# Kernel optimization log

Measured on AMD Instinct MI355X. Metric: run time of the kernel, lower is better.

Reference implementation:

```python
import jax, jax.numpy as jnp
import numpy as np

B, N, K = 32, 8192, 40


def _pi(x, w, b):
    # permute_invariant_layer: subtract per-(sample,feature) max over set dim,
    # then 1x1 conv1d (pointwise matmul over feature dim).
    x = x - jnp.max(x, axis=2, keepdims=True)          # [B, F, N]
    return jnp.einsum('bfn,of->bon', x, w) + b[None, :, None]


def setup_inputs() -> dict:
    key = jax.random.key(0)
    ks = jax.random.split(key, 12)
    def glorot(k, shape, fan_in):
        return jax.random.normal(k, shape, jnp.float32) * (1.0 / np.sqrt(fan_in))
    return {
        'x': jax.random.normal(ks[0], (B, 3, N), jnp.float32),
        'w1': glorot(ks[1], (64, 3), 3),   'b1': jnp.zeros((64,), jnp.float32),
        'w2': glorot(ks[2], (128, 64), 64), 'b2': jnp.zeros((128,), jnp.float32),
        'w3': glorot(ks[3], (256, 128), 128), 'b3': jnp.zeros((256,), jnp.float32),
        'fc1_w': glorot(ks[4], (128, 256), 256), 'fc1_b': jnp.zeros((128,), jnp.float32),
        'fc2_w': glorot(ks[5], (K, 128), 128),   'fc2_b': jnp.zeros((K,), jnp.float32),
    }


def reference(x, w1, b1, w2, b2, w3, b3, fc1_w, fc1_b, fc2_w, fc2_b):
    h = jnp.tanh(_pi(x, w1, b1))          # [B, 64, N]
    h = jnp.tanh(_pi(h, w2, b2))          # [B, 128, N]
    h = jnp.tanh(_pi(h, w3, b3))          # [B, 256, N]
    g = jnp.max(h, axis=2)                # global max pool -> [B, 256]
    # dropout omitted (deterministic/eval reference)
    g = jnp.tanh(g @ fc1_w.T + fc1_b)     # [B, 128]
    g = jnp.tanh(g @ fc2_w.T + fc2_b)     # [B, K]
    return jax.nn.log_softmax(g, axis=-1)
```

## Files before the change

kernel.cpp:

```cpp
#include <hip/hip_runtime.h>
#include <hip/hip_bf16.h>

#define B_  32
#define N_  8192
#define C1  64
#define C2  128
#define C3  256
#define KO  40
#define SLOTS 8

typedef __attribute__((ext_vector_type(8))) short bh8;
typedef __attribute__((ext_vector_type(4))) float f32x4;

union FragU { uint u[4]; bh8 h; uint4 v; };

#define MFMA_BF16 __builtin_amdgcn_mfma_f32_16x16x32_bf16


__device__ __forceinline__ float ftanh(float x) {
    float e = __expf(2.0f * x);
    float r = __builtin_amdgcn_rcpf(e + 1.0f);
    return fmaf(-2.0f, r, 1.0f);
}

__device__ __forceinline__ float quadMax(float v) {
    v = fmaxf(v, __shfl_xor(v, 1, 64));
    v = fmaxf(v, __shfl_xor(v, 2, 64));
    v = fmaxf(v, __shfl_xor(v, 4, 64));
    v = fmaxf(v, __shfl_xor(v, 8, 64));
    return v;
}

__device__ __forceinline__ unsigned encf(float f) {
    unsigned u = __float_as_uint(f);
    return (u & 0x80000000u) ? ~u : (u | 0x80000000u);
}
__device__ __forceinline__ float decf(unsigned e) {
    return __uint_as_float((e & 0x80000000u) ? (e & 0x7fffffffu) : ~e);
}

__device__ __forceinline__ unsigned packbf(float a, float b) {
    __hip_bfloat162 p = __float22bfloat162_rn(make_float2(a, b));
    unsigned u;
    __builtin_memcpy(&u, &p, 4);
    return u;
}


__global__ __launch_bounds__(128) void k_scan(const float* __restrict__ x,
                                              const float* __restrict__ w1,
                                              const float* __restrict__ w2,
                                              const float* __restrict__ w3,
                                              float* __restrict__ mx1p,
                                              float* __restrict__ mx2p,
                                              uint4* __restrict__ w2f,
                                              uint4* __restrict__ w3f,
                                              unsigned* __restrict__ zeroBase) {
    int t = threadIdx.x;
    int bid = blockIdx.x;
    if (bid < 256) {
        int b = bid >> 3, s = bid & 7;
        const float* xb = x + (size_t)b * 3 * N_ + s * 1024 + t;
        float x0[8], x1[8], x2[8];
#pragma unroll
        for (int i = 0; i < 8; ++i) {
            x0[i] = xb[i * 128];
            x1[i] = xb[N_ + i * 128];
            x2[i] = xb[2 * N_ + i * 128];
        }
        float c0 = x0[0], c1 = x1[0], c2 = x2[0];
#pragma unroll
        for (int i = 1; i < 8; ++i) {
            c0 = fmaxf(c0, x0[i]);
            c1 = fmaxf(c1, x1[i]);
            c2 = fmaxf(c2, x2[i]);
        }
        __shared__ float tl[67][132];
#pragma unroll
        for (int o = 0; o < C1; ++o) {
            float w0 = w1[o * 3 + 0], wa = w1[o * 3 + 1], wb = w1[o * 3 + 2];
            float m = -1e30f;
#pragma unroll
            for (int i = 0; i < 8; ++i)
                m = fmaxf(m, fmaf(x0[i], w0, fmaf(x1[i], wa, x2[i] * wb)));
            tl[o][t] = m;
        }
        tl[64][t] = c0;
        tl[65][t] = c1;
        tl[66][t] = c2;
        __syncthreads();
        if (t < 67) {
            const float4* row = (const float4*)&tl[t][0];
            float4 a0 = row[0], a1 = row[1], a2 = row[2], a3 = row[3];
#pragma unroll
            for (int j = 4; j < 32; j += 4) {
                float4 r0 = row[j], r1 = row[j + 1], r2 = row[j + 2], r3 = row[j + 3];
                a0.x = fmaxf(a0.x, r0.x); a0.y = fmaxf(a0.y, r0.y);
                a0.z = fmaxf(a0.z, r0.z); a0.w = fmaxf(a0.w, r0.w);
                a1.x = fmaxf(a1.x, r1.x); a1.y = fmaxf(a1.y, r1.y);
                a1.z = fmaxf(a1.z, r1.z); a1.w = fmaxf(a1.w, r1.w);
                a2.x = fmaxf(a2.x, r2.x); a2.y = fmaxf(a2.y, r2.y);
                a2.z = fmaxf(a2.z, r2.z); a2.w = fmaxf(a2.w, r2.w);
                a3.x = fmaxf(a3.x, r3.x); a3.y = fmaxf(a3.y, r3.y);
                a3.z = fmaxf(a3.z, r3.z); a3.w = fmaxf(a3.w, r3.w);
            }
            float m = fmaxf(fmaxf(fmaxf(a0.x, a0.y), fmaxf(a0.z, a0.w)),
                            fmaxf(fmaxf(a1.x, a1.y), fmaxf(a1.z, a1.w)));
            m = fmaxf(m, fmaxf(fmaxf(a2.x, a2.y), fmaxf(a2.z, a2.w)));
            m = fmaxf(m, fmaxf(fmaxf(a3.x, a3.y), fmaxf(a3.z, a3.w)));
            if (t < 64) mx2p[(s * 32 + b) * 64 + t] = m;
            else        mx1p[(s * 32 + b) * 4 + (t - 64)] = m;
        }
    } else if (bid < 296) {
        int tid = (bid - 256) * 128 + t;
        const float* src;
        uint4* dst;
        if (tid < 1024) {
            int lane = tid & 63, ks = (tid >> 6) & 1, mt = tid >> 7;
            src = w2 + (mt * 16 + (lane & 15)) * C1 + ks * 32 + (lane >> 4) * 8;
            dst = w2f + tid;
        } else {
            int fj = tid - 1024;
            int lane = fj & 63, ks = (fj >> 6) & 3, mt = fj >> 8;
            src = w3 + (mt * 16 + (lane & 15)) * C2 + ks * 32 + (lane >> 4) * 8;
            dst = w3f + fj;
        }
        uint4 o;
        o.x = packbf(src[0], src[1]);
        o.y = packbf(src[2], src[3]);
        o.z = packbf(src[4], src[5]);
        o.w = packbf(src[6], src[7]);
        *dst = o;
    } else {
        int idx = (bid - 296) * 128 + t;
        for (int i = idx; i < 8192 + 4096; i += 256) zeroBase[i] = 0u;
    }
}


__global__ __launch_bounds__(512) void k_passD(const float* __restrict__ x,
                                               const float* __restrict__ w1,
                                               const float* __restrict__ b1,
                                               const float* __restrict__ w2,
                                               const float* __restrict__ b2,
                                               const float* __restrict__ mx1p,
                                               const float* __restrict__ mx2p,
                                               const uint4* __restrict__ w2f,
                                               const uint4* __restrict__ w3f,
                                               unsigned* __restrict__ mx3e,
                                               unsigned* __restrict__ genc) {
    __shared__ uint4 h1v[8][130];
    __shared__ uint2 h2u[32][130];
    __shared__ float w1s[192];
    __shared__ float beff1s[C1];
    __shared__ float m2s[C1];
    __shared__ float beff2s[C2];

    int b = blockIdx.x >> 5;
    int chunk = blockIdx.x & 31;
    int t = threadIdx.x;
    int p = t & 127, hh = t >> 7;
    int lane = t & 63, wv = t >> 6, qd = lane >> 4, ln = lane & 15;

    const float* xbase = x + (size_t)b * 3 * N_ + chunk * 256 + p;
    float xq0[2], xq1[2], xq2[2];
#pragma unroll
    for (int tile = 0; tile < 2; ++tile) {
        xq0[tile] = xbase[tile * 128];
        xq1[tile] = xbase[N_ + tile * 128];
        xq2[tile] = xbase[2 * N_ + tile * 128];
    }

    if (t < 192) w1s[t] = w1[t];
    if (t < C1) {
        float mraw = -1e30f;
#pragma unroll
        for (int s = 0; s < SLOTS; ++s)
            mraw = fmaxf(mraw, mx2p[(s * 32 + b) * 64 + t]);
        float s0 = -1e30f, s1 = -1e30f, s2 = -1e30f;
#pragma unroll
        for (int s = 0; s < SLOTS; ++s) {
            s0 = fmaxf(s0, mx1p[(s * 32 + b) * 4 + 0]);
            s1 = fmaxf(s1, mx1p[(s * 32 + b) * 4 + 1]);
            s2 = fmaxf(s2, mx1p[(s * 32 + b) * 4 + 2]);
        }
        float be = b1[t] - s0 * w1[t * 3 + 0] - s1 * w1[t * 3 + 1]
                         - s2 * w1[t * 3 + 2];
        beff1s[t] = be;
        m2s[t] = ftanh(mraw + be);
    }
    bh8 wf2[2];
    bh8 wf3[2][4];
#pragma unroll
    for (int ks = 0; ks < 2; ++ks) {
        FragU fu;
        fu.v = w2f[(wv * 2 + ks) * 64 + lane];
        wf2[ks] = fu.h;
    }
#pragma unroll
    for (int mi = 0; mi < 2; ++mi)
#pragma unroll
        for (int ks = 0; ks < 4; ++ks) {
            FragU fu;
            fu.v = w3f[((2 * wv + mi) * 4 + ks) * 64 + lane];
            wf3[mi][ks] = fu.h;
        }
    __syncthreads();

    if (t < C2) {
        float a = b2[t];
#pragma unroll 8
        for (int f = 0; f < C1; ++f) a -= m2s[f] * w2[t * C1 + f];
        beff2s[t] = a;
    }

    float vmax2[4];
    float vmax3[2][4];
#pragma unroll
    for (int r = 0; r < 4; ++r) vmax2[r] = -1e30f;
#pragma unroll
    for (int mi = 0; mi < 2; ++mi)
#pragma unroll
        for (int r = 0; r < 4; ++r) vmax3[mi][r] = -1e30f;
    f32x4 bb2;
    bool haveBb2 = false;

    for (int tile = 0; tile < 2; ++tile) {
        float x0 = xq0[tile], x1 = xq1[tile], x2 = xq2[tile];
#pragma unroll
        for (int qq = 0; qq < 2; ++qq) {
            int c = hh * 16 + qq * 8;
            float v[8];
#pragma unroll
            for (int s = 0; s < 8; ++s) {
                float a = beff1s[c + s];
                a = fmaf(x0, w1s[(c + s) * 3 + 0], a);
                a = fmaf(x1, w1s[(c + s) * 3 + 1], a);
                a = fmaf(x2, w1s[(c + s) * 3 + 2], a);
                v[s] = ftanh(a);
            }
            uint4 pk;
            pk.x = packbf(v[0], v[1]);
            pk.y = packbf(v[2], v[3]);
            pk.z = packbf(v[4], v[5]);
            pk.w = packbf(v[6], v[7]);
            h1v[hh * 2 + qq][p] = pk;
        }
        __syncthreads();

        if (!haveBb2) {
#pragma unroll
            for (int r = 0; r < 4; ++r)
                bb2[r] = beff2s[wv * 16 + qd * 4 + r];
            haveBb2 = true;
        }

        for (int nb = 0; nb < 8; ++nb) {
            int n = nb * 16 + ln;
            f32x4 acc = bb2;
#pragma unroll
            for (int ks = 0; ks < 2; ++ks) {
                FragU fb;
                fb.v = h1v[ks * 4 + qd][n];
                acc = MFMA_BF16(wf2[ks], fb.h, acc, 0, 0, 0);
            }
#pragma unroll
            for (int r = 0; r < 4; ++r)
                vmax2[r] = fmaxf(vmax2[r], acc[r]);
            h2u[wv * 4 + qd][n] = make_uint2(packbf(ftanh(acc[0]), ftanh(acc[1])),
                                            packbf(ftanh(acc[2]), ftanh(acc[3])));
        }
        __syncthreads();

        for (int nb = 0; nb < 8; ++nb) {
            int n = nb * 16 + ln;
            f32x4 acc[2];
#pragma unroll
            for (int mi = 0; mi < 2; ++mi) acc[mi] = (f32x4){0.f, 0.f, 0.f, 0.f};
#pragma unroll
            for (int ks = 0; ks < 4; ++ks) {
                int kk = ks * 4 + qd;
                uint2 u0 = h2u[2 * kk][n], u1 = h2u[2 * kk + 1][n];
                FragU fb;
                fb.u[0] = u0.x; fb.u[1] = u0.y; fb.u[2] = u1.x; fb.u[3] = u1.y;
#pragma unroll
                for (int mi = 0; mi < 2; ++mi)
                    acc[mi] = MFMA_BF16(wf3[mi][ks], fb.h, acc[mi], 0, 0, 0);
            }
#pragma unroll
            for (int mi = 0; mi < 2; ++mi)
#pragma unroll
                for (int r = 0; r < 4; ++r)
                    vmax3[mi][r] = fmaxf(vmax3[mi][r], acc[mi][r]);
        }
    }

#pragma unroll
    for (int r = 0; r < 4; ++r) {
        float v = quadMax(vmax2[r]);
        if (ln == 0)
            atomicMax(&mx3e[b * C2 + wv * 16 + qd * 4 + r], encf(v));
    }
#pragma unroll
    for (int mi = 0; mi < 2; ++mi)
#pragma unroll
        for (int r = 0; r < 4; ++r) {
            float v = quadMax(vmax3[mi][r]);
            if (ln == 0)
                atomicMax(&genc[b * C3 + (2 * wv + mi) * 16 + qd * 4 + r], encf(v));
        }
}


__global__ __launch_bounds__(256) void k_fc(const unsigned* __restrict__ mx3e,
                                            const unsigned* __restrict__ genc,
                                            const float* __restrict__ w3,
                                            const float* __restrict__ b3,
                                            const float* __restrict__ fc1w,
                                            const float* __restrict__ fc1b,
                                            const float* __restrict__ fc2w,
                                            const float* __restrict__ fc2b,
                                            float* __restrict__ out) {
    __shared__ float m3[C2];
    __shared__ float gs[C3];
    __shared__ float hs[C2];
    __shared__ float vs[KO];
    __shared__ float red[2];
    int b = blockIdx.x, t = threadIdx.x;
    if (t < C2) m3[t] = ftanh(decf(mx3e[b * C2 + t]));
    __syncthreads();
    {
        float a = b3[t];
#pragma unroll 8
        for (int f = 0; f < C2; ++f) a -= m3[f] * w3[t * C2 + f];
        gs[t] = ftanh(decf(genc[b * C3 + t]) + a);
    }
    __syncthreads();
    if (t < C2) {
        float a = fc1b[t];
#pragma unroll 8
        for (int i = 0; i < C3; ++i) a = fmaf(gs[i], fc1w[t * C3 + i], a);
        hs[t] = ftanh(a);
    }
    __syncthreads();
    if (t < KO) {
        float a = fc2b[t];
#pragma unroll 8
        for (int i = 0; i < C2; ++i) a = fmaf(hs[i], fc2w[t * C2 + i], a);
        vs[t] = ftanh(a);
    }
    __syncthreads();
    if (t == 0) {
        float m = -1e30f;
        for (int j = 0; j < KO; ++j) m = fmaxf(m, vs[j]);
        float s = 0.0f;
        for (int j = 0; j < KO; ++j) s += __expf(vs[j] - m);
        red[0] = m;
        red[1] = __logf(s);
    }
    __syncthreads();
    if (t < KO) out[b * KO + t] = vs[t] - red[0] - red[1];
}


extern "C" void kernel_launch(void* const* d_in, const int* in_sizes, int n_in,
                              void* d_out, int out_size, void* d_ws, size_t ws_size,
                              hipStream_t stream) {
    const float* x    = (const float*)d_in[0];
    const float* w1   = (const float*)d_in[1];
    const float* b1   = (const float*)d_in[2];
    const float* w2   = (const float*)d_in[3];
    const float* b2   = (const float*)d_in[4];
    const float* w3   = (const float*)d_in[5];
    const float* b3   = (const float*)d_in[6];
    const float* fc1w = (const float*)d_in[7];
    const float* fc1b = (const float*)d_in[8];
    const float* fc2w = (const float*)d_in[9];
    const float* fc2b = (const float*)d_in[10];
    float* out = (float*)d_out;

    float* W = (float*)d_ws;
    unsigned* genc = (unsigned*)W;
    unsigned* mx3e = (unsigned*)(W + 8192);
    float*    mx1p = W + 12288;
    float*    mx2p = W + 13312;
    uint4*    w2f  = (uint4*)(W + 29696);
    uint4*    w3f  = (uint4*)(W + 33792);

    k_scan<<<298, 128, 0, stream>>>(x, w1, w2, w3, mx1p, mx2p, w2f, w3f, genc);
    k_passD<<<B_ * 32, 512, 0, stream>>>(x, w1, b1, w2, b2,
                                         mx1p, mx2p, w2f, w3f, mx3e, genc);
    k_fc<<<B_, 256, 0, stream>>>(mx3e, genc, w3, b3, fc1w, fc1b, fc2w, fc2b, out);
}
```

Measured before the change: 148.6 us.

## Fold scan pass into main kernel and replace atomics with per-chunk partial maxima

After: 231.3 us. 1.56x slower.

```diff
diff --git a/kernel.cpp b/kernel.cpp
--- a/kernel.cpp
+++ b/kernel.cpp
@@ -7,7 +7,6 @@
 #define C2  128
 #define C3  256
 #define KO  40
-#define SLOTS 8
 
 typedef __attribute__((ext_vector_type(8))) short bh8;
 typedef __attribute__((ext_vector_type(4))) float f32x4;
@@ -23,6 +22,15 @@
     return fmaf(-2.0f, r, 1.0f);
 }
 
+__device__ __forceinline__ float waveMax(float v) {
+    v = fmaxf(v, __shfl_xor(v, 32, 64));
+    v = fmaxf(v, __shfl_xor(v, 16, 64));
+    v = fmaxf(v, __shfl_xor(v, 8, 64));
+    v = fmaxf(v, __shfl_xor(v, 4, 64));
+    v = fmaxf(v, __shfl_xor(v, 2, 64));
+    v = fmaxf(v, __shfl_xor(v, 1, 64));
+    return v;
+}
 __device__ __forceinline__ float quadMax(float v) {
     v = fmaxf(v, __shfl_xor(v, 1, 64));
     v = fmaxf(v, __shfl_xor(v, 2, 64));
@@ -31,14 +39,6 @@
     return v;
 }
 
-__device__ __forceinline__ unsigned encf(float f) {
-    unsigned u = __float_as_uint(f);
-    return (u & 0x80000000u) ? ~u : (u | 0x80000000u);
-}
-__device__ __forceinline__ float decf(unsigned e) {
-    return __uint_as_float((e & 0x80000000u) ? (e & 0x7fffffffu) : ~e);
-}
-
 __device__ __forceinline__ unsigned packbf(float a, float b) {
     __hip_bfloat162 p = __float22bfloat162_rn(make_float2(a, b));
     unsigned u;
@@ -46,95 +46,15 @@
     return u;
 }
 
-
-__global__ __launch_bounds__(128) void k_scan(const float* __restrict__ x,
-                                              const float* __restrict__ w1,
-                                              const float* __restrict__ w2,
-                                              const float* __restrict__ w3,
-                                              float* __restrict__ mx1p,
-                                              float* __restrict__ mx2p,
-                                              uint4* __restrict__ w2f,
-                                              uint4* __restrict__ w3f,
-                                              unsigned* __restrict__ zeroBase) {
-    int t = threadIdx.x;
-    int bid = blockIdx.x;
-    if (bid < 256) {
-        int b = bid >> 3, s = bid & 7;
-        const float* xb = x + (size_t)b * 3 * N_ + s * 1024 + t;
-        float x0[8], x1[8], x2[8];
-#pragma unroll
-        for (int i = 0; i < 8; ++i) {
-            x0[i] = xb[i * 128];
-            x1[i] = xb[N_ + i * 128];
-            x2[i] = xb[2 * N_ + i * 128];
-        }
-        float c0 = x0[0], c1 = x1[0], c2 = x2[0];
-#pragma unroll
-        for (int i = 1; i < 8; ++i) {
-            c0 = fmaxf(c0, x0[i]);
-            c1 = fmaxf(c1, x1[i]);
-            c2 = fmaxf(c2, x2[i]);
-        }
-        __shared__ float tl[67][132];
-#pragma unroll
-        for (int o = 0; o < C1; ++o) {
-            float w0 = w1[o * 3 + 0], wa = w1[o * 3 + 1], wb = w1[o * 3 + 2];
-            float m = -1e30f;
-#pragma unroll
-            for (int i = 0; i < 8; ++i)
-                m = fmaxf(m, fmaf(x0[i], w0, fmaf(x1[i], wa, x2[i] * wb)));
-            tl[o][t] = m;
-        }
-        tl[64][t] = c0;
-        tl[65][t] = c1;
-        tl[66][t] = c2;
-        __syncthreads();
-        if (t < 67) {
-            const float4* row = (const float4*)&tl[t][0];
-            float4 a0 = row[0], a1 = row[1], a2 = row[2], a3 = row[3];
-#pragma unroll
-            for (int j = 4; j < 32; j += 4) {
-                float4 r0 = row[j], r1 = row[j + 1], r2 = row[j + 2], r3 = row[j + 3];
-                a0.x = fmaxf(a0.x, r0.x); a0.y = fmaxf(a0.y, r0.y);
-                a0.z = fmaxf(a0.z, r0.z); a0.w = fmaxf(a0.w, r0.w);
-                a1.x = fmaxf(a1.x, r1.x); a1.y = fmaxf(a1.y, r1.y);
-                a1.z = fmaxf(a1.z, r1.z); a1.w = fmaxf(a1.w, r1.w);
-                a2.x = fmaxf(a2.x, r2.x); a2.y = fmaxf(a2.y, r2.y);
-                a2.z = fmaxf(a2.z, r2.z); a2.w = fmaxf(a2.w, r2.w);
-                a3.x = fmaxf(a3.x, r3.x); a3.y = fmaxf(a3.y, r3.y);
-                a3.z = fmaxf(a3.z, r3.z); a3.w = fmaxf(a3.w, r3.w);
-            }
-            float m = fmaxf(fmaxf(fmaxf(a0.x, a0.y), fmaxf(a0.z, a0.w)),
-                            fmaxf(fmaxf(a1.x, a1.y), fmaxf(a1.z, a1.w)));
-            m = fmaxf(m, fmaxf(fmaxf(a2.x, a2.y), fmaxf(a2.z, a2.w)));
-            m = fmaxf(m, fmaxf(fmaxf(a3.x, a3.y), fmaxf(a3.z, a3.w)));
-            if (t < 64) mx2p[(s * 32 + b) * 64 + t] = m;
-            else        mx1p[(s * 32 + b) * 4 + (t - 64)] = m;
-        }
-    } else if (bid < 296) {
-        int tid = (bid - 256) * 128 + t;
-        const float* src;
-        uint4* dst;
-        if (tid < 1024) {
-            int lane = tid & 63, ks = (tid >> 6) & 1, mt = tid >> 7;
-            src = w2 + (mt * 16 + (lane & 15)) * C1 + ks * 32 + (lane >> 4) * 8;
-            dst = w2f + tid;
-        } else {
-            int fj = tid - 1024;
-            int lane = fj & 63, ks = (fj >> 6) & 3, mt = fj >> 8;
-            src = w3 + (mt * 16 + (lane & 15)) * C2 + ks * 32 + (lane >> 4) * 8;
-            dst = w3f + fj;
-        }
-        uint4 o;
-        o.x = packbf(src[0], src[1]);
-        o.y = packbf(src[2], src[3]);
-        o.z = packbf(src[4], src[5]);
-        o.w = packbf(src[6], src[7]);
-        *dst = o;
-    } else {
-        int idx = (bid - 296) * 128 + t;
-        for (int i = idx; i < 8192 + 4096; i += 256) zeroBase[i] = 0u;
-    }
+__device__ __forceinline__ bh8 mkfrag(const float* src) {
+    float4 lo = *(const float4*)(src);
+    float4 hi = *(const float4*)(src + 4);
+    FragU fu;
+    fu.u[0] = packbf(lo.x, lo.y);
+    fu.u[1] = packbf(lo.z, lo.w);
+    fu.u[2] = packbf(hi.x, hi.y);
+    fu.u[3] = packbf(hi.z, hi.w);
+    return fu.h;
 }
 
 
@@ -143,12 +63,9 @@
                                                const float* __restrict__ b1,
                                                const float* __restrict__ w2,
                                                const float* __restrict__ b2,
-                                               const float* __restrict__ mx1p,
-                                               const float* __restrict__ mx2p,
-                                               const uint4* __restrict__ w2f,
-                                               const uint4* __restrict__ w3f,
-                                               unsigned* __restrict__ mx3e,
-                                               unsigned* __restrict__ genc) {
+                                               const float* __restrict__ w3,
+                                               float* __restrict__ mx3p,
+                                               float* __restrict__ gencp) {
     __shared__ uint4 h1v[8][130];
     __shared__ uint2 h2u[32][130];
     __shared__ float w1s[192];
@@ -162,6 +79,81 @@
     int p = t & 127, hh = t >> 7;
     int lane = t & 63, wv = t >> 6, qd = lane >> 4, ln = lane & 15;
 
+    if (t < 192) w1s[t] = w1[t];
+
+    {
+        float* redC = (float*)&h2u[0][0];
+        const float* xs = x + (size_t)b * 3 * N_;
+        float sx0[16], sx1[16], sx2[16];
+#pragma unroll
+        for (int i = 0; i < 16; ++i) {
+            sx0[i] = xs[t + i * 512];
+            sx1[i] = xs[N_ + t + i * 512];
+            sx2[i] = xs[2 * N_ + t + i * 512];
+        }
+        float c0 = sx0[0], c1 = sx1[0], c2 = sx2[0];
+#pragma unroll
+        for (int i = 1; i < 16; ++i) {
+            c0 = fmaxf(c0, sx0[i]);
+            c1 = fmaxf(c1, sx1[i]);
+            c2 = fmaxf(c2, sx2[i]);
+        }
+        c0 = waveMax(c0); c1 = waveMax(c1); c2 = waveMax(c2);
+        if (lane == 0) {
+            redC[wv * 68 + 64] = c0;
+            redC[wv * 68 + 65] = c1;
+            redC[wv * 68 + 66] = c2;
+        }
+        float myCh = -1e30f;
+#pragma unroll
+        for (int o = 0; o < C1; ++o) {
+            float w0 = w1[o * 3 + 0], wa = w1[o * 3 + 1], wb = w1[o * 3 + 2];
+            float m = -1e30f;
+#pragma unroll
+            for (int i = 0; i < 16; ++i)
+                m = fmaxf(m, fmaf(sx0[i], w0, fmaf(sx1[i], wa, sx2[i] * wb)));
+            m = waveMax(m);
+            if (lane == o) myCh = m;
+        }
+        redC[wv * 68 + lane] = myCh;
+    }
+    __syncthreads();
+
+    bh8 wf2[2];
+    bh8 wf3[2][4];
+#pragma unroll
+    for (int ks = 0; ks < 2; ++ks)
+        wf2[ks] = mkfrag(w2 + (wv * 16 + ln) * C1 + ks * 32 + qd * 8);
+#pragma unroll
+    for (int mi = 0; mi < 2; ++mi)
+#pragma unroll
+        for (int ks = 0; ks < 4; ++ks)
+            wf3[mi][ks] = mkfrag(w3 + ((2 * wv + mi) * 16 + ln) * C2 + ks * 32 + qd * 8);
+
+    if (t < C1) {
+        const float* redC = (const float*)&h2u[0][0];
+        float mraw = -1e30f, s0 = -1e30f, s1 = -1e30f, s2 = -1e30f;
+#pragma unroll
+        for (int w = 0; w < 8; ++w) {
+            mraw = fmaxf(mraw, redC[w * 68 + t]);
+            s0 = fmaxf(s0, redC[w * 68 + 64]);
+            s1 = fmaxf(s1, redC[w * 68 + 65]);
+            s2 = fmaxf(s2, redC[w * 68 + 66]);
+        }
+        float be = b1[t] - s0 * w1[t * 3 + 0] - s1 * w1[t * 3 + 1]
+                         - s2 * w1[t * 3 + 2];
+        beff1s[t] = be;
+        m2s[t] = ftanh(mraw + be);
+    }
+    __syncthreads();
+
+    if (t < C2) {
+        float a = b2[t];
+#pragma unroll 8
+        for (int f = 0; f < C1; ++f) a -= m2s[f] * w2[t * C1 + f];
+        beff2s[t] = a;
+    }
+
     const float* xbase = x + (size_t)b * 3 * N_ + chunk * 256 + p;
     float xq0[2], xq1[2], xq2[2];
 #pragma unroll
@@ -169,49 +161,6 @@
         xq0[tile] = xbase[tile * 128];
         xq1[tile] = xbase[N_ + tile * 128];
         xq2[tile] = xbase[2 * N_ + tile * 128];
-    }
-
-    if (t < 192) w1s[t] = w1[t];
-    if (t < C1) {
-        float mraw = -1e30f;
-#pragma unroll
-        for (int s = 0; s < SLOTS; ++s)
-            mraw = fmaxf(mraw, mx2p[(s * 32 + b) * 64 + t]);
-        float s0 = -1e30f, s1 = -1e30f, s2 = -1e30f;
-#pragma unroll
-        for (int s = 0; s < SLOTS; ++s) {
-            s0 = fmaxf(s0, mx1p[(s * 32 + b) * 4 + 0]);
-            s1 = fmaxf(s1, mx1p[(s * 32 + b) * 4 + 1]);
-            s2 = fmaxf(s2, mx1p[(s * 32 + b) * 4 + 2]);
-        }
-        float be = b1[t] - s0 * w1[t * 3 + 0] - s1 * w1[t * 3 + 1]
-                         - s2 * w1[t * 3 + 2];
-        beff1s[t] = be;
-        m2s[t] = ftanh(mraw + be);
-    }
-    bh8 wf2[2];
-    bh8 wf3[2][4];
-#pragma unroll
-    for (int ks = 0; ks < 2; ++ks) {
-        FragU fu;
-        fu.v = w2f[(wv * 2 + ks) * 64 + lane];
-        wf2[ks] = fu.h;
-    }
-#pragma unroll
-    for (int mi = 0; mi < 2; ++mi)
-#pragma unroll
-        for (int ks = 0; ks < 4; ++ks) {
-            FragU fu;
-            fu.v = w3f[((2 * wv + mi) * 4 + ks) * 64 + lane];
-            wf3[mi][ks] = fu.h;
-        }
-    __syncthreads();
-
-    if (t < C2) {
-        float a = b2[t];
-#pragma unroll 8
-        for (int f = 0; f < C1; ++f) a -= m2s[f] * w2[t * C1 + f];
-        beff2s[t] = a;
     }
 
     float vmax2[4];
@@ -295,25 +244,24 @@
         }
     }
 
+    int slot = chunk * 32 + b;
 #pragma unroll
     for (int r = 0; r < 4; ++r) {
         float v = quadMax(vmax2[r]);
-        if (ln == 0)
-            atomicMax(&mx3e[b * C2 + wv * 16 + qd * 4 + r], encf(v));
+        if (ln == 0) mx3p[slot * C2 + wv * 16 + qd * 4 + r] = v;
     }
 #pragma unroll
     for (int mi = 0; mi < 2; ++mi)
 #pragma unroll
         for (int r = 0; r < 4; ++r) {
             float v = quadMax(vmax3[mi][r]);
-            if (ln == 0)
-                atomicMax(&genc[b * C3 + (2 * wv + mi) * 16 + qd * 4 + r], encf(v));
-        }
-}
-
-
-__global__ __launch_bounds__(256) void k_fc(const unsigned* __restrict__ mx3e,
-                                            const unsigned* __restrict__ genc,
+            if (ln == 0) gencp[slot * C3 + (2 * wv + mi) * 16 + qd * 4 + r] = v;
+        }
+}
+
+
+__global__ __launch_bounds__(256) void k_fc(const float* __restrict__ mx3p,
+                                            const float* __restrict__ gencp,
                                             const float* __restrict__ w3,
                                             const float* __restrict__ b3,
                                             const float* __restrict__ fc1w,
@@ -327,13 +275,23 @@
     __shared__ float vs[KO];
     __shared__ float red[2];
     int b = blockIdx.x, t = threadIdx.x;
-    if (t < C2) m3[t] = ftanh(decf(mx3e[b * C2 + t]));
+    if (t < C2) {
+        float m = -1e30f;
+#pragma unroll 8
+        for (int c = 0; c < 32; ++c)
+            m = fmaxf(m, mx3p[(c * 32 + b) * C2 + t]);
+        m3[t] = ftanh(m);
+    }
     __syncthreads();
     {
+        float g = -1e30f;
+#pragma unroll 8
+        for (int c = 0; c < 32; ++c)
+            g = fmaxf(g, gencp[(c * 32 + b) * C3 + t]);
         float a = b3[t];
 #pragma unroll 8
         for (int f = 0; f < C2; ++f) a -= m3[f] * w3[t * C2 + f];
-        gs[t] = ftanh(decf(genc[b * C3 + t]) + a);
+        gs[t] = ftanh(g + a);
     }
     __syncthreads();
     if (t < C2) {
@@ -380,15 +338,9 @@
     float* out = (float*)d_out;
 
     float* W = (float*)d_ws;
-    unsigned* genc = (unsigned*)W;
-    unsigned* mx3e = (unsigned*)(W + 8192);
-    float*    mx1p = W + 12288;
-    float*    mx2p = W + 13312;
-    uint4*    w2f  = (uint4*)(W + 29696);
-    uint4*    w3f  = (uint4*)(W + 33792);
-
-    k_scan<<<298, 128, 0, stream>>>(x, w1, w2, w3, mx1p, mx2p, w2f, w3f, genc);
-    k_passD<<<B_ * 32, 512, 0, stream>>>(x, w1, b1, w2, b2,
-                                         mx1p, mx2p, w2f, w3f, mx3e, genc);
-    k_fc<<<B_, 256, 0, stream>>>(mx3e, genc, w3, b3, fc1w, fc1b, fc2w, fc2b, out);
-}
+    float* gencp = W;
+    float* mx3p  = W + 262144;
+
+    k_passD<<<B_ * 32, 512, 0, stream>>>(x, w1, b1, w2, b2, w3, mx3p, gencp);
+    k_fc<<<B_, 256, 0, stream>>>(mx3p, gencp, w3, b3, fc1w, fc1b, fc2w, fc2b, out);
+}
```
